# Performance work log

Measured on AMD Instinct MI355X. Metric: run time of the kernel, lower is better.

Reference implementation:

```python
import jax, jax.numpy as jnp
import numpy as np

D_K = 64
SCALE = 1.0 / (D_K ** 0.5)
NEG = -1.0e9

def setup_inputs() -> dict:
    key = jax.random.key(0)
    kq, kk, kv, km = jax.random.split(key, 4)
    B, H, S, D = 4, 16, 2048, D_K
    query = jax.random.normal(kq, (B, H, S, D), dtype=jnp.float32)
    k_ = jax.random.normal(kk, (B, H, S, D), dtype=jnp.float32)
    v_ = jax.random.normal(kv, (B, H, S, D), dtype=jnp.float32)
    mask = jax.random.randint(km, (B, 1, S, S), 0, 2, dtype=jnp.int32)
    return {"query": query, "key": k_, "value": v_, "mask": mask}

def reference(query, key, value, mask):
    # scores: [B, H, S, S]
    scores = jnp.einsum('bhqd,bhkd->bhqk', query, key) * SCALE
    scores = jnp.where(mask == 0, NEG, scores)
    attn = jax.nn.softmax(scores, axis=-1)
    return jnp.einsum('bhqk,bhkd->bhqd', attn, value)
```

## Files before the change

### kernel.cpp

```cpp
#include <hip/hip_runtime.h>

typedef _Float16 f16x8 __attribute__((ext_vector_type(8)));
typedef _Float16 f16x4 __attribute__((ext_vector_type(4)));
typedef _Float16 f16x2 __attribute__((ext_vector_type(2)));
typedef float    f32x4 __attribute__((ext_vector_type(4)));
typedef float    f32x16 __attribute__((ext_vector_type(16)));
typedef unsigned u32x4 __attribute__((ext_vector_type(4)));
typedef unsigned long long u64;

constexpr int Bc = 4, Hc = 16, Sc = 2048, Dc = 64;
constexpr int KVBLK = 64;
constexpr int NKV = Sc / KVBLK;
constexpr int QB  = 128;
constexpr int NQT = Sc / QB;
constexpr int NQ  = 32;

__device__ __forceinline__ float fast_exp2(float x) {
#if __has_builtin(__builtin_amdgcn_exp2f)
  return __builtin_amdgcn_exp2f(x);
#else
  return exp2f(x);
#endif
}

__device__ __forceinline__ void gload16(const void* g, void* l) {
  __builtin_amdgcn_global_load_lds(
      (const __attribute__((address_space(1))) void*)g,
      (__attribute__((address_space(3))) void*)l, 16, 0, 0);
}

__device__ __forceinline__ f32x16 mfma32(f16x8 a, f16x8 b, f32x16 c) {
  return __builtin_amdgcn_mfma_f32_32x32x16_f16(a, b, c, 0, 0, 0);
}

__device__ __forceinline__ unsigned pkrtz(float x, float y) {
  return __builtin_bit_cast(unsigned, __builtin_amdgcn_cvt_pkrtz(x, y));
}

__device__ __forceinline__ float dot2acc(unsigned pk, float acc) {
#if __has_builtin(__builtin_amdgcn_fdot2)
  const f16x2 one2 = {(_Float16)1.f, (_Float16)1.f};
  return __builtin_amdgcn_fdot2(__builtin_bit_cast(f16x2, pk), one2, acc, false);
#else
  const f16x2 v = __builtin_bit_cast(f16x2, pk);
  return acc + (float)v[0] + (float)v[1];
#endif
}

__device__ __forceinline__ f32x16 zero16() {
  f32x16 z;
  #pragma unroll
  for (int i = 0; i < 16; ++i) z[i] = 0.f;
  return z;
}

__global__ __launch_bounds__(256)
void cvt_k_sw(const float* __restrict__ K, _Float16* __restrict__ Ko) {
  const int tile = blockIdx.x;
  const int t = threadIdx.x;
  const float* src = K + (size_t)tile * 4096;
  _Float16* dst = Ko + (size_t)tile * 4096;
  #pragma unroll
  for (int cc = 0; cc < 2; ++cc) {
    const int c = t + cc * 256;
    const int r = c >> 3, s = c & 7;
    const int ss = s ^ (r & 7);
    const float* p = src + r * 64 + ss * 8;
    const float4 a = *(const float4*)p;
    const float4 b2 = *(const float4*)(p + 4);
    f16x8 h = {(_Float16)a.x, (_Float16)a.y, (_Float16)a.z, (_Float16)a.w,
               (_Float16)b2.x, (_Float16)b2.y, (_Float16)b2.z, (_Float16)b2.w};
    *(f16x8*)(dst + (size_t)c * 8) = h;
  }
}

__global__ __launch_bounds__(256)
void cvt_v_sw2(const float* __restrict__ V, _Float16* __restrict__ Vo) {
  __shared__ float tile[64][65];
  const int tb = blockIdx.x;
  const int t = threadIdx.x;
  const float* src = V + (size_t)tb * 4096;
  {
    const int r = t >> 2, c0 = (t & 3) * 16;
    #pragma unroll
    for (int j = 0; j < 16; j += 4)
      *(float4*)&tile[r][c0 + j] = *(const float4*)(src + r * 64 + c0 + j);
  }
  __syncthreads();
  _Float16* dst = Vo + (size_t)tb * 4096;
  #pragma unroll
  for (int cc = 0; cc < 2; ++cc) {
    const int c = t + cc * 256;
    const int d = c >> 3, cpos = c & 7;
    const int cl = cpos ^ (d & 7);
    f16x8 h;
    #pragma unroll
    for (int e = 0; e < 8; ++e) {
      const int kap = cl * 8 + e;
      const int key = (kap & 51) | ((kap & 4) << 1) | ((kap & 8) >> 1);
      h[e] = (_Float16)tile[key][d];
    }
    *(f16x8*)(dst + (size_t)c * 8) = h;
  }
}

__global__ __launch_bounds__(256)
void pack_mask(const int* __restrict__ M, u64* __restrict__ MB) {
  const int gid  = blockIdx.x * 256 + threadIdx.x;
  const int wv   = gid >> 6, lane = gid & 63;
  const int kv   = wv & (NKV - 1);
  const int row  = (wv >> 5) & (Sc - 1);
  const int b    = wv >> 16;
  const int m    = M[((size_t)b * Sc + row) * Sc + (size_t)kv * 64 + lane];
  const u64 bits = __ballot(m != 0);
  if (lane == 0)
    MB[(((size_t)b * NQ + (row >> 6)) * NKV + kv) * 64 + (row & 63)] = bits;
}

__global__ __launch_bounds__(256, 4)
void attn_fwd8(const float* __restrict__ Q, const _Float16* __restrict__ Ksw,
               const _Float16* __restrict__ Vsw, const u64* __restrict__ MB,
               float* __restrict__ O)
{
  const int bid = (blockIdx.x & 7) * 128 + (blockIdx.x >> 3);
  const int qt  = bid & (NQT - 1);
  const int bh  = bid >> 4;
  const int b   = bh >> 4;
  const int q0  = qt * QB;

  const int tid = threadIdx.x;
  const int w   = tid >> 6;
  const int l   = tid & 63;
  const int q5  = l & 31;
  const int hb  = l >> 5;
  const int xb  = q5 & 7;

  __shared__ _Float16 SB[16384];
  const char* sb = (const char*)SB;

  int as_[4];
  #pragma unroll
  for (int s = 0; s < 4; ++s)
    as_[s] = q5 * 128 + (((((s << 1) | hb)) ^ xb) << 4);

  f16x8 qf[4];
  {
    const float qs = 0.125f * 1.4426950408889634f;
    const float* qr = Q + ((size_t)bh * Sc + q0 + w * 32 + q5) * Dc + 8 * hb;
    #pragma unroll
    for (int s = 0; s < 4; ++s) {
      const float4 f0 = *(const float4*)(qr + s * 16);
      const float4 f1 = *(const float4*)(qr + s * 16 + 4);
      f16x8 t = {(_Float16)(f0.x * qs), (_Float16)(f0.y * qs),
                 (_Float16)(f0.z * qs), (_Float16)(f0.w * qs),
                 (_Float16)(f1.x * qs), (_Float16)(f1.y * qs),
                 (_Float16)(f1.z * qs), (_Float16)(f1.w * qs)};
      qf[s] = t;
    }
  }

  f32x16 o0 = zero16(), o1 = zero16();
  float l_acc = 0.f;
  const float NEGL = -1.4426950e9f;

  const char* KswT = (const char*)(Ksw + (size_t)bh * Sc * Dc);
  const char* VswT = (const char*)(Vsw + (size_t)bh * Sc * Dc);
  const int row = q0 + w * 32 + q5;
  const u64* Mb = MB + ((size_t)(b * NQ + (row >> 6)) * NKV) * 64 + (row & 63);

  auto stage = [&](int kvt, int buf) {
    const char* g = (w < 2) ? KswT + (size_t)kvt * 8192 + (w & 1) * 4096
                            : VswT + (size_t)kvt * 8192 + (w & 1) * 4096;
    char* lb = (char*)SB + buf * 16384 + ((w < 2) ? 0 : 8192) + (w & 1) * 4096;
    #pragma unroll
    for (int j = 0; j < 4; ++j)
      gload16(g + j * 1024 + l * 16, lb + j * 1024);
  };

  auto body = [&](int buf, u64 mbits) {
    const int base = buf * 16384;
    f32x16 acc0 = zero16(), acc1 = zero16();
    __builtin_amdgcn_s_setprio(1);
    #pragma unroll
    for (int s = 0; s < 4; ++s) {
      const f16x8 k0 = *(const f16x8*)(sb + base + as_[s]);
      acc0 = mfma32(k0, qf[s], acc0);
    }
    #pragma unroll
    for (int s = 0; s < 4; ++s) {
      const f16x8 k1 = *(const f16x8*)(sb + base + 4096 + as_[s]);
      acc1 = mfma32(k1, qf[s], acc1);
    }
    __builtin_amdgcn_s_setprio(0);

    u32x4 pw0, pw1, pw2, pw3;
    {
      const unsigned mh = (unsigned)mbits;
      #pragma unroll
      for (int b2 = 0; b2 < 4; ++b2) {
        const unsigned nib = (mh >> (8 * b2 + 4 * hb)) & 0xFu;
        #pragma unroll
        for (int a2 = 0; a2 < 4; ++a2) {
          const int r = 4 * b2 + a2;
          acc0[r] = fast_exp2(((nib >> a2) & 1u) ? acc0[r] : NEGL);
        }
      }
      #pragma unroll
      for (int i = 0; i < 4; ++i) {
        pw0[i] = pkrtz(acc0[2 * i], acc0[2 * i + 1]);
        pw1[i] = pkrtz(acc0[8 + 2 * i], acc0[8 + 2 * i + 1]);
        l_acc = dot2acc(pw0[i], l_acc);
        l_acc = dot2acc(pw1[i], l_acc);
      }
    }
    {
      const unsigned mh = (unsigned)(mbits >> 32);
      #pragma unroll
      for (int b2 = 0; b2 < 4; ++b2) {
        const unsigned nib = (mh >> (8 * b2 + 4 * hb)) & 0xFu;
        #pragma unroll
        for (int a2 = 0; a2 < 4; ++a2) {
          const int r = 4 * b2 + a2;
          acc1[r] = fast_exp2(((nib >> a2) & 1u) ? acc1[r] : NEGL);
        }
      }
      #pragma unroll
      for (int i = 0; i < 4; ++i) {
        pw2[i] = pkrtz(acc1[2 * i], acc1[2 * i + 1]);
        pw3[i] = pkrtz(acc1[8 + 2 * i], acc1[8 + 2 * i + 1]);
        l_acc = dot2acc(pw2[i], l_acc);
        l_acc = dot2acc(pw3[i], l_acc);
      }
    }
    const f16x8 pa0 = __builtin_bit_cast(f16x8, pw0);
    const f16x8 pa1 = __builtin_bit_cast(f16x8, pw1);
    const f16x8 pa2 = __builtin_bit_cast(f16x8, pw2);
    const f16x8 pa3 = __builtin_bit_cast(f16x8, pw3);

    __builtin_amdgcn_s_setprio(1);
    o0 = mfma32(pa0, *(const f16x8*)(sb + base + 8192 + as_[0]), o0);
    o0 = mfma32(pa1, *(const f16x8*)(sb + base + 8192 + as_[1]), o0);
    o0 = mfma32(pa2, *(const f16x8*)(sb + base + 8192 + as_[2]), o0);
    o0 = mfma32(pa3, *(const f16x8*)(sb + base + 8192 + as_[3]), o0);
    o1 = mfma32(pa0, *(const f16x8*)(sb + base + 12288 + as_[0]), o1);
    o1 = mfma32(pa1, *(const f16x8*)(sb + base + 12288 + as_[1]), o1);
    o1 = mfma32(pa2, *(const f16x8*)(sb + base + 12288 + as_[2]), o1);
    o1 = mfma32(pa3, *(const f16x8*)(sb + base + 12288 + as_[3]), o1);
    __builtin_amdgcn_s_setprio(0);
  };

  u64 mb_next = Mb[0];
  stage(0, 0);
  __syncthreads();
  for (int kv = 0; kv < NKV; kv += 2) {
    const u64 mb0 = mb_next;
    const u64 mb1 = Mb[(size_t)(kv + 1) * 64];
    stage(kv + 1, 1);
    body(0, mb0);
    __syncthreads();
    if (kv + 2 < NKV) {
      mb_next = Mb[(size_t)(kv + 2) * 64];
      stage(kv + 2, 0);
    }
    body(1, mb1);
    __syncthreads();
  }

  l_acc += __shfl_xor(l_acc, 32, 64);
  #pragma unroll
  for (int reg = 0; reg < 16; ++reg) {
    const int qrow = (reg & 3) + 8 * (reg >> 2) + 4 * hb;
    const float li = 1.0f / __shfl(l_acc, qrow, 64);
    float* op = O + ((size_t)bh * Sc + q0 + w * 32 + qrow) * Dc + q5;
    op[0]  = o0[reg] * li;
    op[32] = o1[reg] * li;
  }
}

constexpr int LDSW = KVBLK + 8;

__global__ __launch_bounds__(256)
void attn_fwd_v1(const float* __restrict__ Q, const float* __restrict__ K,
                 const float* __restrict__ V, const int* __restrict__ M,
                 float* __restrict__ O)
{
  const int bid   = blockIdx.x;
  const int qtile = bid & 31;
  const int bh    = bid >> 5;
  const int b     = bh >> 4;

  const float* Qp = Q + ((size_t)bh * Sc + (size_t)qtile * 64) * Dc;
  const float* Kp = K + (size_t)bh * Sc * Dc;
  const float* Vp = V + (size_t)bh * Sc * Dc;
  const int*   Mp = M + (size_t)b * Sc * Sc + (size_t)qtile * 64 * Sc;
  float*       Op = O + ((size_t)bh * Sc + (size_t)qtile * 64) * Dc;

  __shared__ _Float16 Klds [KVBLK][LDSW];
  __shared__ _Float16 Vtlds[Dc]   [LDSW];
  __shared__ _Float16 Pl   [64]   [LDSW];

  const int tid = threadIdx.x;
  const int w   = tid >> 6;
  const int l   = tid & 63;
  const int lg  = l >> 4;
  const int lc  = l & 15;

  f16x8 qf[2];
  {
    const float qs = 0.125f * 1.4426950408889634f;
    const float* qrow = Qp + (size_t)(w * 16 + lc) * Dc + 8 * lg;
    #pragma unroll
    for (int ks = 0; ks < 2; ++ks) {
      f16x8 t;
      #pragma unroll
      for (int e = 0; e < 8; ++e) t[e] = (_Float16)(qrow[ks * 32 + e] * qs);
      qf[ks] = t;
    }
  }

  f32x4 o_acc[4];
  #pragma unroll
  for (int nt = 0; nt < 4; ++nt) o_acc[nt] = (f32x4){0.f, 0.f, 0.f, 0.f};
  float m_r[4], l_r[4];
  #pragma unroll
  for (int r = 0; r < 4; ++r) { m_r[r] = -3.0e38f; l_r[r] = 0.f; }
  const float NEGL = -1.4426950e9f;

  for (int kv = 0; kv < NKV; ++kv) {
    const float* Kt = Kp + (size_t)kv * KVBLK * Dc;
    const float* Vt = Vp + (size_t)kv * KVBLK * Dc;
    __syncthreads();
    {
      const int r = tid >> 2, c0 = (tid & 3) * 16;
      const float* src = Kt + (size_t)r * Dc + c0;
      f16x8 h0, h1;
      #pragma unroll
      for (int e = 0; e < 8; ++e) h0[e] = (_Float16)src[e];
      #pragma unroll
      for (int e = 0; e < 8; ++e) h1[e] = (_Float16)src[8 + e];
      *(f16x8*)&Klds[r][c0]     = h0;
      *(f16x8*)&Klds[r][c0 + 8] = h1;
    }
    {
      const int r0 = (tid >> 4) * 4, c0 = (tid & 15) * 4;
      float a_[4][4];
      #pragma unroll
      for (int i = 0; i < 4; ++i) {
        const float4 v4 = *(const float4*)(Vt + (size_t)(r0 + i) * Dc + c0);
        a_[i][0] = v4.x; a_[i][1] = v4.y; a_[i][2] = v4.z; a_[i][3] = v4.w;
      }
      #pragma unroll
      for (int j = 0; j < 4; ++j) {
        f16x4 t = {(_Float16)a_[0][j], (_Float16)a_[1][j],
                   (_Float16)a_[2][j], (_Float16)a_[3][j]};
        *(f16x4*)&Vtlds[c0 + j][r0] = t;
      }
    }
    __syncthreads();

    f32x4 s_acc[4];
    #pragma unroll
    for (int nt = 0; nt < 4; ++nt) {
      f32x4 acc = (f32x4){0.f, 0.f, 0.f, 0.f};
      #pragma unroll
      for (int ks = 0; ks < 2; ++ks) {
        f16x8 kf = *(const f16x8*)&Klds[nt * 16 + lc][ks * 32 + 8 * lg];
        acc = __builtin_amdgcn_mfma_f32_16x16x32_f16(qf[ks], kf, acc, 0, 0, 0);
      }
      s_acc[nt] = acc;
    }

    const int* mbase = Mp + (size_t)kv * KVBLK + lc;
    #pragma unroll
    for (int r = 0; r < 4; ++r) {
      const int qrow = w * 16 + 4 * lg + r;
      const int* mr = mbase + (size_t)qrow * Sc;
      float s0 = (mr[0]  != 0) ? s_acc[0][r] : NEGL;
      float s1 = (mr[16] != 0) ? s_acc[1][r] : NEGL;
      float s2 = (mr[32] != 0) ? s_acc[2][r] : NEGL;
      float s3 = (mr[48] != 0) ? s_acc[3][r] : NEGL;
      float mx = fmaxf(fmaxf(s0, s1), fmaxf(s2, s3));
      #pragma unroll
      for (int off = 1; off < 16; off <<= 1)
        mx = fmaxf(mx, __shfl_xor(mx, off, 64));
      const float mn   = fmaxf(m_r[r], mx);
      const float corr = fast_exp2(m_r[r] - mn);
      m_r[r] = mn;
      float p0 = fast_exp2(s0 - mn);
      float p1 = fast_exp2(s1 - mn);
      float p2 = fast_exp2(s2 - mn);
      float p3 = fast_exp2(s3 - mn);
      float rs = (p0 + p1) + (p2 + p3);
      #pragma unroll
      for (int off = 1; off < 16; off <<= 1)
        rs += __shfl_xor(rs, off, 64);
      l_r[r] = l_r[r] * corr + rs;
      #pragma unroll
      for (int nt = 0; nt < 4; ++nt) o_acc[nt][r] *= corr;
      Pl[qrow][lc]      = (_Float16)p0;
      Pl[qrow][16 + lc] = (_Float16)p1;
      Pl[qrow][32 + lc] = (_Float16)p2;
      Pl[qrow][48 + lc] = (_Float16)p3;
    }

    #pragma unroll
    for (int nt = 0; nt < 4; ++nt) {
      #pragma unroll
      for (int ks = 0; ks < 2; ++ks) {
        f16x8 pf = *(const f16x8*)&Pl[w * 16 + lc][ks * 32 + 8 * lg];
        f16x8 vf = *(const f16x8*)&Vtlds[nt * 16 + lc][ks * 32 + 8 * lg];
        o_acc[nt] = __builtin_amdgcn_mfma_f32_16x16x32_f16(pf, vf, o_acc[nt], 0, 0, 0);
      }
    }
  }

  #pragma unroll
  for (int r = 0; r < 4; ++r) {
    const float inv = 1.0f / l_r[r];
    float* orow = Op + (size_t)(w * 16 + 4 * lg + r) * Dc;
    #pragma unroll
    for (int nt = 0; nt < 4; ++nt)
      orow[nt * 16 + lc] = o_acc[nt][r] * inv;
  }
}

extern "C" void kernel_launch(void* const* d_in, const int* in_sizes, int n_in,
                              void* d_out, int out_size, void* d_ws, size_t ws_size,
                              hipStream_t stream) {
  (void)in_sizes; (void)n_in; (void)out_size;
  const float* Q = (const float*)d_in[0];
  const float* K = (const float*)d_in[1];
  const float* V = (const float*)d_in[2];
  const int*   M = (const int*)d_in[3];
  float*       O = (float*)d_out;

  const size_t nKV      = (size_t)Bc * Hc * Sc * Dc;
  const size_t bytesK16 = nKV * 2;
  const size_t bytesMB  = (size_t)Bc * NQ * NKV * 64 * 8;
  const size_t need     = 2 * bytesK16 + bytesMB;

  if (ws_size >= need) {
    _Float16* K16  = (_Float16*)d_ws;
    _Float16* Vt16 = (_Float16*)((char*)d_ws + bytesK16);
    u64*      MBp  = (u64*)((char*)d_ws + 2 * bytesK16);
    hipLaunchKernelGGL(cvt_k_sw,   dim3(2048),  dim3(256), 0, stream, K, K16);
    hipLaunchKernelGGL(cvt_v_sw2,  dim3(2048),  dim3(256), 0, stream, V, Vt16);
    hipLaunchKernelGGL(pack_mask,  dim3(65536), dim3(256), 0, stream, M, MBp);
    hipLaunchKernelGGL(attn_fwd8,  dim3(1024),  dim3(256), 0, stream, Q, K16, Vt16, MBp, O);
  } else {
    hipLaunchKernelGGL(attn_fwd_v1, dim3(2048), dim3(256), 0, stream, Q, K, V, M, O);
  }
}
```

Measured before the change: 136.4 us.

## Split each KV tile across two waves per query group with LDS output reduction

Doubles the block to 512 threads (8 waves) so each pair of waves shares one 32-row query group and splits the 64-key tile into two 32-key halves. Each wave does half the QK and PV MFMAs and half the exp work, which shortens the per-tile critical path and raises the wave count per CU. At the end, partial O accumulators and row sums are reduced through LDS before normalisation. The cost is a larger LDS footprint, extra barriers, and a reduction epilogue, with more register pressure under the new launch bounds.

```diff
diff --git a/kernel.cpp b/kernel.cpp
--- a/kernel.cpp
+++ b/kernel.cpp
@@ -117,8 +117,8 @@
     MB[(((size_t)b * NQ + (row >> 6)) * NKV + kv) * 64 + (row & 63)] = bits;
 }
 
-__global__ __launch_bounds__(256, 4)
-void attn_fwd8(const float* __restrict__ Q, const _Float16* __restrict__ Ksw,
+__global__ __launch_bounds__(512, 6)
+void attn_fwd9(const float* __restrict__ Q, const _Float16* __restrict__ Ksw,
                const _Float16* __restrict__ Vsw, const u64* __restrict__ MB,
                float* __restrict__ O)
 {
@@ -130,12 +130,14 @@
 
   const int tid = threadIdx.x;
   const int w   = tid >> 6;
+  const int g   = w >> 1;
+  const int kt  = w & 1;
   const int l   = tid & 63;
   const int q5  = l & 31;
   const int hb  = l >> 5;
   const int xb  = q5 & 7;
 
-  __shared__ _Float16 SB[16384];
+  __shared__ _Float16 SB[16384 + 256];
   const char* sb = (const char*)SB;
 
   int as_[4];
@@ -146,7 +148,7 @@
   f16x8 qf[4];
   {
     const float qs = 0.125f * 1.4426950408889634f;
-    const float* qr = Q + ((size_t)bh * Sc + q0 + w * 32 + q5) * Dc + 8 * hb;
+    const float* qr = Q + ((size_t)bh * Sc + q0 + g * 32 + q5) * Dc + 8 * hb;
     #pragma unroll
     for (int s = 0; s < 4; ++s) {
       const float4 f0 = *(const float4*)(qr + s * 16);
@@ -160,92 +162,60 @@
   }
 
   f32x16 o0 = zero16(), o1 = zero16();
-  float l_acc = 0.f;
+  float la = 0.f, lb_ = 0.f;
   const float NEGL = -1.4426950e9f;
 
   const char* KswT = (const char*)(Ksw + (size_t)bh * Sc * Dc);
   const char* VswT = (const char*)(Vsw + (size_t)bh * Sc * Dc);
-  const int row = q0 + w * 32 + q5;
+  const int row = q0 + g * 32 + q5;
   const u64* Mb = MB + ((size_t)(b * NQ + (row >> 6)) * NKV) * 64 + (row & 63);
 
   auto stage = [&](int kvt, int buf) {
-    const char* g = (w < 2) ? KswT + (size_t)kvt * 8192 + (w & 1) * 4096
-                            : VswT + (size_t)kvt * 8192 + (w & 1) * 4096;
-    char* lb = (char*)SB + buf * 16384 + ((w < 2) ? 0 : 8192) + (w & 1) * 4096;
-    #pragma unroll
-    for (int j = 0; j < 4; ++j)
-      gload16(g + j * 1024 + l * 16, lb + j * 1024);
+    const char* gp = (w < 4) ? KswT + (size_t)kvt * 8192 + w * 2048
+                             : VswT + (size_t)kvt * 8192 + (w - 4) * 2048;
+    char* lbp = (char*)SB + buf * 16384 + ((w < 4) ? w * 2048 : 8192 + (w - 4) * 2048);
+    gload16(gp + l * 16, lbp);
+    gload16(gp + 1024 + l * 16, lbp + 1024);
   };
 
   auto body = [&](int buf, u64 mbits) {
     const int base = buf * 16384;
-    f32x16 acc0 = zero16(), acc1 = zero16();
+    const int kbase = base + kt * 4096;
+    f32x16 acc = zero16();
     __builtin_amdgcn_s_setprio(1);
-    #pragma unroll
-    for (int s = 0; s < 4; ++s) {
-      const f16x8 k0 = *(const f16x8*)(sb + base + as_[s]);
-      acc0 = mfma32(k0, qf[s], acc0);
-    }
-    #pragma unroll
-    for (int s = 0; s < 4; ++s) {
-      const f16x8 k1 = *(const f16x8*)(sb + base + 4096 + as_[s]);
-      acc1 = mfma32(k1, qf[s], acc1);
-    }
+    acc = mfma32(*(const f16x8*)(sb + kbase + as_[0]), qf[0], acc);
+    acc = mfma32(*(const f16x8*)(sb + kbase + as_[1]), qf[1], acc);
+    acc = mfma32(*(const f16x8*)(sb + kbase + as_[2]), qf[2], acc);
+    acc = mfma32(*(const f16x8*)(sb + kbase + as_[3]), qf[3], acc);
     __builtin_amdgcn_s_setprio(0);
 
-    u32x4 pw0, pw1, pw2, pw3;
-    {
-      const unsigned mh = (unsigned)mbits;
-      #pragma unroll
-      for (int b2 = 0; b2 < 4; ++b2) {
-        const unsigned nib = (mh >> (8 * b2 + 4 * hb)) & 0xFu;
-        #pragma unroll
-        for (int a2 = 0; a2 < 4; ++a2) {
-          const int r = 4 * b2 + a2;
-          acc0[r] = fast_exp2(((nib >> a2) & 1u) ? acc0[r] : NEGL);
-        }
+    const unsigned mh = (unsigned)(mbits >> (32 * kt));
+    #pragma unroll
+    for (int b2 = 0; b2 < 4; ++b2) {
+      const unsigned nib = (mh >> (8 * b2 + 4 * hb)) & 0xFu;
+      #pragma unroll
+      for (int a2 = 0; a2 < 4; ++a2) {
+        const int r = 4 * b2 + a2;
+        acc[r] = fast_exp2(((nib >> a2) & 1u) ? acc[r] : NEGL);
       }
-      #pragma unroll
-      for (int i = 0; i < 4; ++i) {
-        pw0[i] = pkrtz(acc0[2 * i], acc0[2 * i + 1]);
-        pw1[i] = pkrtz(acc0[8 + 2 * i], acc0[8 + 2 * i + 1]);
-        l_acc = dot2acc(pw0[i], l_acc);
-        l_acc = dot2acc(pw1[i], l_acc);
-      }
-    }
-    {
-      const unsigned mh = (unsigned)(mbits >> 32);
-      #pragma unroll
-      for (int b2 = 0; b2 < 4; ++b2) {
-        const unsigned nib = (mh >> (8 * b2 + 4 * hb)) & 0xFu;
-        #pragma unroll
-        for (int a2 = 0; a2 < 4; ++a2) {
-          const int r = 4 * b2 + a2;
-          acc1[r] = fast_exp2(((nib >> a2) & 1u) ? acc1[r] : NEGL);
-        }
-      }
-      #pragma unroll
-      for (int i = 0; i < 4; ++i) {
-        pw2[i] = pkrtz(acc1[2 * i], acc1[2 * i + 1]);
-        pw3[i] = pkrtz(acc1[8 + 2 * i], acc1[8 + 2 * i + 1]);
-        l_acc = dot2acc(pw2[i], l_acc);
-        l_acc = dot2acc(pw3[i], l_acc);
-      }
+    }
+    u32x4 pw0, pw1;
+    #pragma unroll
+    for (int i = 0; i < 4; ++i) {
+      pw0[i] = pkrtz(acc[2 * i], acc[2 * i + 1]);
+      pw1[i] = pkrtz(acc[8 + 2 * i], acc[8 + 2 * i + 1]);
+      la  = dot2acc(pw0[i], la);
+      lb_ = dot2acc(pw1[i], lb_);
     }
     const f16x8 pa0 = __builtin_bit_cast(f16x8, pw0);
     const f16x8 pa1 = __builtin_bit_cast(f16x8, pw1);
-    const f16x8 pa2 = __builtin_bit_cast(f16x8, pw2);
-    const f16x8 pa3 = __builtin_bit_cast(f16x8, pw3);
-
+
+    const int s0 = 2 * kt, s1 = 2 * kt + 1;
     __builtin_amdgcn_s_setprio(1);
-    o0 = mfma32(pa0, *(const f16x8*)(sb + base + 8192 + as_[0]), o0);
-    o0 = mfma32(pa1, *(const f16x8*)(sb + base + 8192 + as_[1]), o0);
-    o0 = mfma32(pa2, *(const f16x8*)(sb + base + 8192 + as_[2]), o0);
-    o0 = mfma32(pa3, *(const f16x8*)(sb + base + 8192 + as_[3]), o0);
-    o1 = mfma32(pa0, *(const f16x8*)(sb + base + 12288 + as_[0]), o1);
-    o1 = mfma32(pa1, *(const f16x8*)(sb + base + 12288 + as_[1]), o1);
-    o1 = mfma32(pa2, *(const f16x8*)(sb + base + 12288 + as_[2]), o1);
-    o1 = mfma32(pa3, *(const f16x8*)(sb + base + 12288 + as_[3]), o1);
+    o0 = mfma32(pa0, *(const f16x8*)(sb + base + 8192 + as_[s0]), o0);
+    o0 = mfma32(pa1, *(const f16x8*)(sb + base + 8192 + as_[s1]), o0);
+    o1 = mfma32(pa0, *(const f16x8*)(sb + base + 12288 + as_[s0]), o1);
+    o1 = mfma32(pa1, *(const f16x8*)(sb + base + 12288 + as_[s1]), o1);
     __builtin_amdgcn_s_setprio(0);
   };
 
@@ -266,14 +236,35 @@
     __syncthreads();
   }
 
-  l_acc += __shfl_xor(l_acc, 32, 64);
-  #pragma unroll
-  for (int reg = 0; reg < 16; ++reg) {
-    const int qrow = (reg & 3) + 8 * (reg >> 2) + 4 * hb;
-    const float li = 1.0f / __shfl(l_acc, qrow, 64);
-    float* op = O + ((size_t)bh * Sc + q0 + w * 32 + qrow) * Dc + q5;
-    op[0]  = o0[reg] * li;
-    op[32] = o1[reg] * li;
+  float lsum = la + lb_;
+  lsum += __shfl_xor(lsum, 32, 64);
+
+  float* xch = (float*)SB;
+  float* lx  = (float*)(SB + 16384);
+  __syncthreads();
+  if (kt == 1) {
+    float* dst = xch + ((g * 64 + l) << 5);
+    #pragma unroll
+    for (int i = 0; i < 4; ++i) {
+      *(float4*)(dst + 4 * i)      = float4{o0[4*i], o0[4*i+1], o0[4*i+2], o0[4*i+3]};
+      *(float4*)(dst + 16 + 4 * i) = float4{o1[4*i], o1[4*i+1], o1[4*i+2], o1[4*i+3]};
+    }
+    if (hb == 0) lx[g * 32 + q5] = lsum;
+  }
+  __syncthreads();
+  if (kt == 0) {
+    const float* src = xch + ((g * 64 + l) << 5);
+    #pragma unroll
+    for (int i = 0; i < 16; ++i) { o0[i] += src[i]; o1[i] += src[16 + i]; }
+    const float lt = lsum + lx[g * 32 + q5];
+    #pragma unroll
+    for (int reg = 0; reg < 16; ++reg) {
+      const int qrow = (reg & 3) + 8 * (reg >> 2) + 4 * hb;
+      const float li = 1.0f / __shfl(lt, qrow, 64);
+      float* op = O + ((size_t)bh * Sc + q0 + g * 32 + qrow) * Dc + q5;
+      op[0]  = o0[reg] * li;
+      op[32] = o1[reg] * li;
+    }
   }
 }
 
@@ -446,7 +437,7 @@
     hipLaunchKernelGGL(cvt_k_sw,   dim3(2048),  dim3(256), 0, stream, K, K16);
     hipLaunchKernelGGL(cvt_v_sw2,  dim3(2048),  dim3(256), 0, stream, V, Vt16);
     hipLaunchKernelGGL(pack_mask,  dim3(65536), dim3(256), 0, stream, M, MBp);
-    hipLaunchKernelGGL(attn_fwd8,  dim3(1024),  dim3(256), 0, stream, Q, K16, Vt16, MBp, O);
+    hipLaunchKernelGGL(attn_fwd9,  dim3(1024),  dim3(512), 0, stream, Q, K16, Vt16, MBp, O);
   } else {
     hipLaunchKernelGGL(attn_fwd_v1, dim3(2048), dim3(256), 0, stream, Q, K, V, M, O);
   }
```

Result: slower. 316.0 us (+131.7%).
